# Kernel tuning notes

Measured on AMD Instinct MI355X. Metric: run time of the kernel, lower is better.

The kernel has to match this reference:

```python
import jax, jax.numpy as jnp
import numpy as np

# Static graph-batch configuration (equal-size graphs so per-graph top-k is static)
B = 256          # number of graphs in the batch
N = 400          # nodes per graph
D = 256          # in_dim
DEG = 32         # average degree
E = B * N * DEG  # total edges
RATIO = 0.5
K = int(np.ceil(RATIO * N))  # nodes kept per graph by mytopk
NT = B * N


def setup_inputs() -> dict:
    key = jax.random.key(0)
    k1, k2, k3, k4 = jax.random.split(key, 4)
    feature = jax.random.normal(k1, (NT, D), dtype=jnp.float32)
    W = jax.random.normal(k2, (D, 1), dtype=jnp.float32) * (1.0 / np.sqrt(D))
    b = jnp.zeros((1,), dtype=jnp.float32)
    # edges stay within each graph: global id = graph_offset + local id
    g = jnp.repeat(jnp.arange(B, dtype=jnp.int32), N * DEG)  # [E] graph id per edge
    src = g * N + jax.random.randint(k3, (E,), 0, N, dtype=jnp.int32)
    dst = g * N + jax.random.randint(k4, (E,), 0, N, dtype=jnp.int32)
    return {"feature": feature, "W": W, "b": b, "src": src, "dst": dst}


def _forward(feature, W, b, src, dst):
    # --- GraphConv(in_dim, 1), norm='both' (dgl): h = D_in^-1/2 A D_out^-1/2 (X W) + b
    ones_e = jnp.ones((E,), dtype=feature.dtype)
    deg_out = jax.ops.segment_sum(ones_e, src, num_segments=NT)
    deg_in = jax.ops.segment_sum(ones_e, dst, num_segments=NT)
    norm_out = jnp.maximum(deg_out, 1.0) ** -0.5  # dgl clamps degree to min 1
    norm_in = jnp.maximum(deg_in, 1.0) ** -0.5
    h = (feature @ W) * norm_out[:, None]                      # [NT,1]
    agg = jax.ops.segment_sum(h[src], dst, num_segments=NT)    # [NT,1]
    score = (agg * norm_in[:, None] + b)[:, 0]                 # [NT]

    # --- mytopk: per-graph top-k node selection by score (descending)
    score2d = score.reshape(B, N)
    _, idx = jax.lax.top_k(score2d, K)                         # [B,K] local ids
    offsets = (jnp.arange(B, dtype=jnp.int32) * N)[:, None]
    perm = (idx.astype(jnp.int32) + offsets).reshape(-1)       # [B*K] global ids

    # complement nodes (mask trick in the original): ascending order per graph
    sel = jnp.zeros((NT,), dtype=bool).at[perm].set(True)
    sel2d = sel.reshape(B, N).astype(jnp.int32)
    order = jnp.argsort(sel2d, axis=1, stable=True)[:, : N - K]  # unselected first
    perm_com = (order.astype(jnp.int32) + offsets).reshape(-1)   # [B*(N-K)]

    # --- gated feature gathers
    feature_dis = feature[perm] * jnp.tanh(score[perm])[:, None]
    feature_com = feature[perm_com] * jnp.tanh(score[perm_com])[:, None]

    # --- subgraph structure as static-shape edge masks (dgl.node_subgraph keeps
    #     edges whose both endpoints are selected)
    e_dis_mask = sel[src] & sel[dst]
    e_com_mask = (~sel[src]) & (~sel[dst])

    score_soft = jax.nn.softmax(score, axis=0)  # Softmax(dim=0) over all nodes
    return feature_dis, feature_com, perm, perm_com, score_soft, e_dis_mask, e_com_mask


def reference(feature, W, b, src, dst):
    return _forward(feature, W, b, src, dst)
```

## Files before the change

### kernel.cpp

```cpp
#include <hip/hip_runtime.h>
#include <math.h>

#define B_    256
#define N_    400
#define D_    256
#define EPG_  12800
#define E_    3276800
#define NT_   102400
#define K_    200
#define NKC_  200
#define QB_   1024
#define EPQ_  3200

#define O_FDIS 0
#define O_FCOM 13107200
#define O_PERM 26214400
#define O_PCOM 26265600
#define O_SOFT 26316800
#define O_EDIS 26419200
#define O_ECOM 29696000

#define NEG_INF (-3.402823466e38f)

typedef float nfv4 __attribute__((ext_vector_type(4)));
static __device__ __forceinline__ void nt_store4(float4* p, float4 v) {
    nfv4 x; x.x = v.x; x.y = v.y; x.z = v.z; x.w = v.w;
    __builtin_nontemporal_store(x, (nfv4*)p);
}

__global__ __launch_bounds__(256) void k_A(const float* __restrict__ feat,
                                           const float* __restrict__ W,
                                           const int* __restrict__ src,
                                           const int* __restrict__ dst,
                                           float* __restrict__ hraw,
                                           int* __restrict__ degp_o,
                                           int* __restrict__ degp_i) {
    const int bid = blockIdx.x, tid = threadIdx.x;
    if (bid < NT_ / 16) {
        const int gw   = (bid * 256 + tid) >> 6;
        const int lane = tid & 63;
        const float4 w4 = ((const float4*)W)[lane];
        const int r0 = gw * 4;
        const float4* fb = (const float4*)feat;
        float4 a0 = fb[(size_t)(r0    ) * 64 + lane];
        float4 a1 = fb[(size_t)(r0 + 1) * 64 + lane];
        float4 a2 = fb[(size_t)(r0 + 2) * 64 + lane];
        float4 a3 = fb[(size_t)(r0 + 3) * 64 + lane];
        float d0 = a0.x*w4.x + a0.y*w4.y + a0.z*w4.z + a0.w*w4.w;
        float d1 = a1.x*w4.x + a1.y*w4.y + a1.z*w4.z + a1.w*w4.w;
        float d2 = a2.x*w4.x + a2.y*w4.y + a2.z*w4.z + a2.w*w4.w;
        float d3 = a3.x*w4.x + a3.y*w4.y + a3.z*w4.z + a3.w*w4.w;
        #pragma unroll
        for (int off = 32; off > 0; off >>= 1) {
            d0 += __shfl_down(d0, off, 64);
            d1 += __shfl_down(d1, off, 64);
            d2 += __shfl_down(d2, off, 64);
            d3 += __shfl_down(d3, off, 64);
        }
        if (lane == 0) {
            hraw[r0    ] = d0;
            hraw[r0 + 1] = d1;
            hraw[r0 + 2] = d2;
            hraw[r0 + 3] = d3;
        }
    } else {
        __shared__ int hp[8][N_];
        const int qb = bid - NT_ / 16;
        const int wave = tid >> 6;
        const int nbase = (qb >> 2) * N_;
        for (int t = tid; t < 8 * N_; t += 256) ((int*)hp)[t] = 0;
        __syncthreads();
        int* hw_o = hp[wave * 2 + 0];
        int* hw_i = hp[wave * 2 + 1];
        const int4* s4 = (const int4*)(src + qb * EPQ_);
        const int4* d4 = (const int4*)(dst + qb * EPQ_);
        for (int i = tid; i < EPQ_ / 4; i += 256) {
            int4 s = s4[i]; int4 d = d4[i];
            atomicAdd(&hw_o[s.x - nbase], 1);
            atomicAdd(&hw_o[s.y - nbase], 1);
            atomicAdd(&hw_o[s.z - nbase], 1);
            atomicAdd(&hw_o[s.w - nbase], 1);
            atomicAdd(&hw_i[d.x - nbase], 1);
            atomicAdd(&hw_i[d.y - nbase], 1);
            atomicAdd(&hw_i[d.z - nbase], 1);
            atomicAdd(&hw_i[d.w - nbase], 1);
        }
        __syncthreads();
        for (int t = tid; t < N_; t += 256) {
            degp_o[qb * N_ + t] = hp[0][t] + hp[2][t] + hp[4][t] + hp[6][t];
            degp_i[qb * N_ + t] = hp[1][t] + hp[3][t] + hp[5][t] + hp[7][t];
        }
    }
}

__global__ __launch_bounds__(256) void k_B(const int* __restrict__ src,
                                           const int* __restrict__ dst,
                                           const float* __restrict__ hraw,
                                           const int* __restrict__ degp_o,
                                           float* __restrict__ aggp) {
    __shared__ float hl[N_];
    __shared__ float sp[4][N_];
    const int qb = blockIdx.x, tid = threadIdx.x, wave = tid >> 6;
    const int g = qb >> 2, nbase = g * N_, g4 = g * 4;
    for (int t = tid; t < N_; t += 256) {
        const int dsum = degp_o[(g4 + 0) * N_ + t] + degp_o[(g4 + 1) * N_ + t]
                       + degp_o[(g4 + 2) * N_ + t] + degp_o[(g4 + 3) * N_ + t];
        hl[t] = hraw[nbase + t] * (1.0f / sqrtf(fmaxf((float)dsum, 1.0f)));
    }
    for (int t = tid; t < 4 * N_; t += 256) ((float*)sp)[t] = 0.0f;
    __syncthreads();

    float* spw = sp[wave];
    const int4* s4 = (const int4*)(src + qb * EPQ_);
    const int4* d4 = (const int4*)(dst + qb * EPQ_);
    for (int i = tid; i < EPQ_ / 4; i += 256) {
        int4 s = s4[i]; int4 d = d4[i];
        atomicAdd(&spw[d.x - nbase], hl[s.x - nbase]);
        atomicAdd(&spw[d.y - nbase], hl[s.y - nbase]);
        atomicAdd(&spw[d.z - nbase], hl[s.z - nbase]);
        atomicAdd(&spw[d.w - nbase], hl[s.w - nbase]);
    }
    __syncthreads();
    for (int t = tid; t < N_; t += 256)
        aggp[qb * N_ + t] = sp[0][t] + sp[1][t] + sp[2][t] + sp[3][t];
}

__global__ __launch_bounds__(512) void k_C(const float* __restrict__ aggp,
                                           const int* __restrict__ degp_i,
                                           const float* __restrict__ bp,
                                           float* __restrict__ score,
                                           float* __restrict__ pm,
                                           float* __restrict__ ps,
                                           int* __restrict__ sel,
                                           int* __restrict__ orow,
                                           float* __restrict__ out) {
    __shared__ float scl[N_];
    __shared__ unsigned long long bmask[7];
    const int g = blockIdx.x, tid = threadIdx.x;
    const int wave = tid >> 6, lane = tid & 63;
    const int nbase = g * N_, g4 = g * 4;

    const float bb = bp[0];
    if (tid < N_) {
        const float a = aggp[(g4 + 0) * N_ + tid] + aggp[(g4 + 1) * N_ + tid]
                      + aggp[(g4 + 2) * N_ + tid] + aggp[(g4 + 3) * N_ + tid];
        const int dsum = degp_i[(g4 + 0) * N_ + tid] + degp_i[(g4 + 1) * N_ + tid]
                       + degp_i[(g4 + 2) * N_ + tid] + degp_i[(g4 + 3) * N_ + tid];
        const float v = a * (1.0f / sqrtf(fmaxf((float)dsum, 1.0f))) + bb;
        score[nbase + tid] = v;
        scl[tid] = v;
    }
    __syncthreads();

    bool selb = false;
    if (tid < 448) {
        float sreg[7];
        #pragma unroll
        for (int t = 0; t < 7; ++t) {
            const int j = t * 64 + lane;
            sreg[t] = (j < N_) ? scl[j] : NEG_INF;
        }
        const float v = (tid < N_) ? scl[tid] : NEG_INF;
        int rnk = 0;
        #pragma unroll
        for (int t = 0; t < 7; ++t) {
            #pragma unroll
            for (int l2 = 0; l2 < 64; ++l2) {
                const int j = t * 64 + l2;
                if (j < N_) {
                    const float u = __uint_as_float(
                        __builtin_amdgcn_readlane(__float_as_uint(sreg[t]), l2));
                    rnk += ((u > v) || (u == v && j < tid)) ? 1 : 0;
                }
            }
        }
        selb = (tid < N_) && (rnk < K_);
        if (tid < N_) sel[nbase + tid] = selb ? 1 : 0;
        if (selb) {
            orow[nbase + tid] = g * K_ + rnk;
            out[O_PERM + g * K_ + rnk] = (float)(nbase + tid);
        }
        unsigned long long bal = __ballot(selb);
        if (lane == 0) bmask[wave] = bal;
    }
    if (wave == 7) {
        float m = NEG_INF;
        for (int i = lane; i < N_; i += 64) m = fmaxf(m, scl[i]);
        #pragma unroll
        for (int o = 32; o > 0; o >>= 1) m = fmaxf(m, __shfl_xor(m, o, 64));
        float s = 0.0f;
        for (int i = lane; i < N_; i += 64) s += expf(scl[i] - m);
        #pragma unroll
        for (int o = 32; o > 0; o >>= 1) s += __shfl_xor(s, o, 64);
        if (lane == 0) { pm[g] = m; ps[g] = s; }
    }
    __syncthreads();

    if (tid < N_ && !selb) {
        int nsel = 0;
        #pragma unroll
        for (int w = 0; w < 7; ++w)
            if (w < wave) nsel += (int)__popcll(bmask[w]);
        nsel += (int)__popcll(bmask[wave] & ((1ull << lane) - 1ull));
        const int pos = tid - nsel;
        orow[nbase + tid] = B_ * K_ + g * NKC_ + pos;
        out[O_PCOM + g * NKC_ + pos] = (float)(nbase + tid);
    }
}

__global__ __launch_bounds__(256) void k_D(const float* __restrict__ feat,
                                           const float* __restrict__ score,
                                           const int* __restrict__ orow,
                                           const float* __restrict__ pm,
                                           const float* __restrict__ ps,
                                           const int* __restrict__ src,
                                           const int* __restrict__ dst,
                                           const int* __restrict__ sel,
                                           float* __restrict__ out) {
    const int bid = blockIdx.x, tid = threadIdx.x;
    if (bid < NT_ / 16) {
        __shared__ float sm[4], ss[4];
        const int lane = tid & 63, wv = tid >> 6;
        float m = pm[tid], s = ps[tid];
        #pragma unroll
        for (int o = 32; o > 0; o >>= 1) {
            float mo = __shfl_xor(m, o, 64);
            float so = __shfl_xor(s, o, 64);
            float M2 = fmaxf(m, mo);
            s = s * expf(m - M2) + so * expf(mo - M2);
            m = M2;
        }
        if (lane == 0) { sm[wv] = m; ss[wv] = s; }
        __syncthreads();
        const float M = fmaxf(fmaxf(sm[0], sm[1]), fmaxf(sm[2], sm[3]));
        const float S = ss[0] * expf(sm[0] - M) + ss[1] * expf(sm[1] - M)
                      + ss[2] * expf(sm[2] - M) + ss[3] * expf(sm[3] - M);

        const int gw = (bid * 256 + tid) >> 6;
        const int n0 = gw * 4;
        const float4* fb = (const float4*)feat;
        float4 v0 = fb[(size_t)(n0    ) * 64 + lane];
        float4 v1 = fb[(size_t)(n0 + 1) * 64 + lane];
        float4 v2 = fb[(size_t)(n0 + 2) * 64 + lane];
        float4 v3 = fb[(size_t)(n0 + 3) * 64 + lane];
        float s0 = score[n0], s1 = score[n0 + 1], s2 = score[n0 + 2], s3 = score[n0 + 3];
        int   r0 = orow[n0],  r1 = orow[n0 + 1],  r2 = orow[n0 + 2],  r3 = orow[n0 + 3];
        float t0 = tanhf(s0), t1 = tanhf(s1), t2 = tanhf(s2), t3 = tanhf(s3);
        v0.x *= t0; v0.y *= t0; v0.z *= t0; v0.w *= t0;
        v1.x *= t1; v1.y *= t1; v1.z *= t1; v1.w *= t1;
        v2.x *= t2; v2.y *= t2; v2.z *= t2; v2.w *= t2;
        v3.x *= t3; v3.y *= t3; v3.z *= t3; v3.w *= t3;
        nt_store4(((float4*)(out + (size_t)r0 * D_)) + lane, v0);
        nt_store4(((float4*)(out + (size_t)r1 * D_)) + lane, v1);
        nt_store4(((float4*)(out + (size_t)r2 * D_)) + lane, v2);
        nt_store4(((float4*)(out + (size_t)r3 * D_)) + lane, v3);
        if (lane == 0) {
            out[O_SOFT + n0    ] = expf(s0 - M) / S;
            out[O_SOFT + n0 + 1] = expf(s1 - M) / S;
            out[O_SOFT + n0 + 2] = expf(s2 - M) / S;
            out[O_SOFT + n0 + 3] = expf(s3 - M) / S;
        }
    } else {
        const int i = (bid - NT_ / 16) * 256 + tid;
        int4 s = ((const int4*)src)[i];
        int4 d = ((const int4*)dst)[i];
        int a0 = sel[s.x], a1 = sel[s.y], a2 = sel[s.z], a3 = sel[s.w];
        int b0 = sel[d.x], b1 = sel[d.y], b2 = sel[d.z], b3 = sel[d.w];
        float4 mdis, mcom;
        mdis.x = (a0 & b0) ? 1.0f : 0.0f;  mcom.x = (a0 | b0) ? 0.0f : 1.0f;
        mdis.y = (a1 & b1) ? 1.0f : 0.0f;  mcom.y = (a1 | b1) ? 0.0f : 1.0f;
        mdis.z = (a2 & b2) ? 1.0f : 0.0f;  mcom.z = (a2 | b2) ? 0.0f : 1.0f;
        mdis.w = (a3 & b3) ? 1.0f : 0.0f;  mcom.w = (a3 | b3) ? 0.0f : 1.0f;
        nt_store4(((float4*)(out + O_EDIS)) + i, mdis);
        nt_store4(((float4*)(out + O_ECOM)) + i, mcom);
    }
}

extern "C" void kernel_launch(void* const* d_in, const int* in_sizes, int n_in,
                              void* d_out, int out_size, void* d_ws, size_t ws_size,
                              hipStream_t stream) {
    const float* feat = (const float*)d_in[0];
    const float* W    = (const float*)d_in[1];
    const float* bp   = (const float*)d_in[2];
    const int*   src  = (const int*)d_in[3];
    const int*   dst  = (const int*)d_in[4];
    float* out = (float*)d_out;

    char* ws = (char*)d_ws;
    float* hraw   = (float*)(ws + 0);
    int*   degp_o = (int*)  (ws + 409600);
    int*   degp_i = (int*)  (ws + 2048000);
    float* aggp   = (float*)(ws + 3686400);
    float* score  = (float*)(ws + 5324800);
    int*   sel    = (int*)  (ws + 5734400);
    int*   orow   = (int*)  (ws + 6144000);
    float* pm     = (float*)(ws + 6553600);
    float* ps     = (float*)(ws + 6554624);

    k_A<<<NT_ / 16 + QB_,  256, 0, stream>>>(feat, W, src, dst, hraw, degp_o, degp_i);
    k_B<<<QB_,             256, 0, stream>>>(src, dst, hraw, degp_o, aggp);
    k_C<<<B_,              512, 0, stream>>>(aggp, degp_i, bp, score, pm, ps, sel, orow, out);
    k_D<<<NT_ / 16 + E_ / 4 / 256, 256, 0, stream>>>(feat, score, orow, pm, ps,
                                                     src, dst, sel, out);
}
```

Baseline: 289.2 us.

## Split edge histograms into per-wave slabs and reorder degree blocks first

Degree counting and aggregation now give each wave its own 1600-edge slab with a private LDS histogram written straight to global partials. This removes block-level __syncthreads and the in-block reduction across waves, and doubles the partial count per graph to 8. The histogram blocks are placed before the matvec blocks in k_A so the atomic-heavy work is scheduled first. In exchange the workspace partial buffers double in size and k_B/k_C must sum 8 partials instead of 4.

```diff
diff --git a/kernel.cpp b/kernel.cpp
--- a/kernel.cpp
+++ b/kernel.cpp
@@ -9,8 +9,8 @@
 #define NT_   102400
 #define K_    200
 #define NKC_  200
-#define QB_   1024
-#define EPQ_  3200
+#define NSLAB_ 2048
+#define I4PS_  400
 
 #define O_FDIS 0
 #define O_FCOM 13107200
@@ -36,8 +36,34 @@
                                            int* __restrict__ degp_o,
                                            int* __restrict__ degp_i) {
     const int bid = blockIdx.x, tid = threadIdx.x;
-    if (bid < NT_ / 16) {
-        const int gw   = (bid * 256 + tid) >> 6;
+    if (bid < NSLAB_ / 4) {
+        __shared__ int hp[4][2][N_];
+        const int wave = tid >> 6, lane = tid & 63;
+        const int slab = bid * 4 + wave;
+        const int nbase = (slab >> 3) * N_;
+        int* mo = hp[wave][0];
+        int* mi = hp[wave][1];
+        for (int t = lane; t < N_; t += 64) { mo[t] = 0; mi[t] = 0; }
+        const int4* s4 = (const int4*)src + slab * I4PS_;
+        const int4* d4 = (const int4*)dst + slab * I4PS_;
+        for (int i = lane; i < I4PS_; i += 64) {
+            int4 s = s4[i]; int4 d = d4[i];
+            atomicAdd(&mo[s.x - nbase], 1);
+            atomicAdd(&mo[s.y - nbase], 1);
+            atomicAdd(&mo[s.z - nbase], 1);
+            atomicAdd(&mo[s.w - nbase], 1);
+            atomicAdd(&mi[d.x - nbase], 1);
+            atomicAdd(&mi[d.y - nbase], 1);
+            atomicAdd(&mi[d.z - nbase], 1);
+            atomicAdd(&mi[d.w - nbase], 1);
+        }
+        for (int t = lane; t < N_; t += 64) {
+            degp_o[slab * N_ + t] = mo[t];
+            degp_i[slab * N_ + t] = mi[t];
+        }
+    } else {
+        const int rb = bid - NSLAB_ / 4;
+        const int gw   = (rb * 256 + tid) >> 6;
         const int lane = tid & 63;
         const float4 w4 = ((const float4*)W)[lane];
         const int r0 = gw * 4;
@@ -63,33 +89,6 @@
             hraw[r0 + 2] = d2;
             hraw[r0 + 3] = d3;
         }
-    } else {
-        __shared__ int hp[8][N_];
-        const int qb = bid - NT_ / 16;
-        const int wave = tid >> 6;
-        const int nbase = (qb >> 2) * N_;
-        for (int t = tid; t < 8 * N_; t += 256) ((int*)hp)[t] = 0;
-        __syncthreads();
-        int* hw_o = hp[wave * 2 + 0];
-        int* hw_i = hp[wave * 2 + 1];
-        const int4* s4 = (const int4*)(src + qb * EPQ_);
-        const int4* d4 = (const int4*)(dst + qb * EPQ_);
-        for (int i = tid; i < EPQ_ / 4; i += 256) {
-            int4 s = s4[i]; int4 d = d4[i];
-            atomicAdd(&hw_o[s.x - nbase], 1);
-            atomicAdd(&hw_o[s.y - nbase], 1);
-            atomicAdd(&hw_o[s.z - nbase], 1);
-            atomicAdd(&hw_o[s.w - nbase], 1);
-            atomicAdd(&hw_i[d.x - nbase], 1);
-            atomicAdd(&hw_i[d.y - nbase], 1);
-            atomicAdd(&hw_i[d.z - nbase], 1);
-            atomicAdd(&hw_i[d.w - nbase], 1);
-        }
-        __syncthreads();
-        for (int t = tid; t < N_; t += 256) {
-            degp_o[qb * N_ + t] = hp[0][t] + hp[2][t] + hp[4][t] + hp[6][t];
-            degp_i[qb * N_ + t] = hp[1][t] + hp[3][t] + hp[5][t] + hp[7][t];
-        }
     }
 }
 
@@ -100,29 +99,32 @@
                                            float* __restrict__ aggp) {
     __shared__ float hl[N_];
     __shared__ float sp[4][N_];
-    const int qb = blockIdx.x, tid = threadIdx.x, wave = tid >> 6;
-    const int g = qb >> 2, nbase = g * N_, g4 = g * 4;
+    const int bid = blockIdx.x, tid = threadIdx.x;
+    const int wave = tid >> 6, lane = tid & 63;
+    const int g = bid >> 1, nbase = g * N_, g8 = g * 8;
+
     for (int t = tid; t < N_; t += 256) {
-        const int dsum = degp_o[(g4 + 0) * N_ + t] + degp_o[(g4 + 1) * N_ + t]
-                       + degp_o[(g4 + 2) * N_ + t] + degp_o[(g4 + 3) * N_ + t];
+        int dsum = 0;
+        #pragma unroll
+        for (int q = 0; q < 8; ++q) dsum += degp_o[(g8 + q) * N_ + t];
         hl[t] = hraw[nbase + t] * (1.0f / sqrtf(fmaxf((float)dsum, 1.0f)));
     }
-    for (int t = tid; t < 4 * N_; t += 256) ((float*)sp)[t] = 0.0f;
+    for (int t = lane; t < N_; t += 64) sp[wave][t] = 0.0f;
     __syncthreads();
 
+    const int slab = bid * 4 + wave;
     float* spw = sp[wave];
-    const int4* s4 = (const int4*)(src + qb * EPQ_);
-    const int4* d4 = (const int4*)(dst + qb * EPQ_);
-    for (int i = tid; i < EPQ_ / 4; i += 256) {
+    const int4* s4 = (const int4*)src + slab * I4PS_;
+    const int4* d4 = (const int4*)dst + slab * I4PS_;
+    for (int i = lane; i < I4PS_; i += 64) {
         int4 s = s4[i]; int4 d = d4[i];
         atomicAdd(&spw[d.x - nbase], hl[s.x - nbase]);
         atomicAdd(&spw[d.y - nbase], hl[s.y - nbase]);
         atomicAdd(&spw[d.z - nbase], hl[s.z - nbase]);
         atomicAdd(&spw[d.w - nbase], hl[s.w - nbase]);
     }
-    __syncthreads();
-    for (int t = tid; t < N_; t += 256)
-        aggp[qb * N_ + t] = sp[0][t] + sp[1][t] + sp[2][t] + sp[3][t];
+    for (int t = lane; t < N_; t += 64)
+        aggp[slab * N_ + t] = spw[t];
 }
 
 __global__ __launch_bounds__(512) void k_C(const float* __restrict__ aggp,
@@ -138,14 +140,16 @@
     __shared__ unsigned long long bmask[7];
     const int g = blockIdx.x, tid = threadIdx.x;
     const int wave = tid >> 6, lane = tid & 63;
-    const int nbase = g * N_, g4 = g * 4;
+    const int nbase = g * N_, g8 = g * 8;
 
     const float bb = bp[0];
     if (tid < N_) {
-        const float a = aggp[(g4 + 0) * N_ + tid] + aggp[(g4 + 1) * N_ + tid]
-                      + aggp[(g4 + 2) * N_ + tid] + aggp[(g4 + 3) * N_ + tid];
-        const int dsum = degp_i[(g4 + 0) * N_ + tid] + degp_i[(g4 + 1) * N_ + tid]
-                       + degp_i[(g4 + 2) * N_ + tid] + degp_i[(g4 + 3) * N_ + tid];
+        float a = 0.0f; int dsum = 0;
+        #pragma unroll
+        for (int q = 0; q < 8; ++q) {
+            a    += aggp  [(g8 + q) * N_ + tid];
+            dsum += degp_i[(g8 + q) * N_ + tid];
+        }
         const float v = a * (1.0f / sqrtf(fmaxf((float)dsum, 1.0f))) + bb;
         score[nbase + tid] = v;
         scl[tid] = v;
@@ -289,17 +293,19 @@
     char* ws = (char*)d_ws;
     float* hraw   = (float*)(ws + 0);
     int*   degp_o = (int*)  (ws + 409600);
-    int*   degp_i = (int*)  (ws + 2048000);
-    float* aggp   = (float*)(ws + 3686400);
-    float* score  = (float*)(ws + 5324800);
-    int*   sel    = (int*)  (ws + 5734400);
-    int*   orow   = (int*)  (ws + 6144000);
-    float* pm     = (float*)(ws + 6553600);
-    float* ps     = (float*)(ws + 6554624);
-
-    k_A<<<NT_ / 16 + QB_,  256, 0, stream>>>(feat, W, src, dst, hraw, degp_o, degp_i);
-    k_B<<<QB_,             256, 0, stream>>>(src, dst, hraw, degp_o, aggp);
-    k_C<<<B_,              512, 0, stream>>>(aggp, degp_i, bp, score, pm, ps, sel, orow, out);
+    int*   degp_i = (int*)  (ws + 3686400);
+    float* aggp   = (float*)(ws + 6963200);
+    float* score  = (float*)(ws + 10240000);
+    int*   sel    = (int*)  (ws + 10649600);
+    int*   orow   = (int*)  (ws + 11059200);
+    float* pm     = (float*)(ws + 11468800);
+    float* ps     = (float*)(ws + 11469824);
+
+    k_A<<<NSLAB_ / 4 + NT_ / 16,   256, 0, stream>>>(feat, W, src, dst,
+                                                     hraw, degp_o, degp_i);
+    k_B<<<NSLAB_ / 4,              256, 0, stream>>>(src, dst, hraw, degp_o, aggp);
+    k_C<<<B_,                      512, 0, stream>>>(aggp, degp_i, bp, score,
+                                                     pm, ps, sel, orow, out);
     k_D<<<NT_ / 16 + E_ / 4 / 256, 256, 0, stream>>>(feat, score, orow, pm, ps,
                                                      src, dst, sel, out);
 }
```

After: 291.5 us. About the same (+0.8%).
